# Optimization experiments

Hardware: AMD Instinct MI355X
Metric: run time of the kernel (lower is better)

The kernel has to match this reference:

```python
import jax, jax.numpy as jnp
import numpy as np

B, D, C = 8192, 64, 2048
BETA = 0.25
EPS = 1e-6


def setup_inputs() -> dict:
    key = jax.random.key(0)
    k1, k2, k3 = jax.random.split(key, 3)
    x = jax.random.normal(k1, (B, D), dtype=jnp.float32)
    prev_q = jax.random.normal(k2, (B, D), dtype=jnp.float32)
    codes = jax.random.normal(k3, (1, C, D), dtype=jnp.float32) * 0.1  # learned codebook param
    return {"x": x, "prev_q": prev_q, "codes": codes}


def _rotation_matrix(u, v, eps=EPS):
    # u: (B, D) unit vectors, v: (D,) unit vector. Rodrigues-like rotation mapping v -> u.
    uvT = u[:, :, None] * v[None, None, :]          # (B, D, D)
    vuT = v[None, :, None] * u[:, None, :]          # (B, D, D)
    A = uvT - vuT
    A2 = jnp.einsum('bij,bjk->bik', A, A)
    dot = jnp.sum(u * v[None, :], axis=-1)[:, None, None]  # (B,1,1)
    I = jnp.eye(u.shape[-1], dtype=u.dtype)
    return I[None] + A + A2 / (1.0 + dot + eps)


def reference(x, prev_q, codes):
    # F.normalize(prev_q, dim=-1, eps=1e-6)
    norm = jnp.linalg.norm(prev_q, axis=-1, keepdims=True)
    u = prev_q / jnp.maximum(norm, EPS)
    v = jnp.full((D,), 1.0 / float(D) ** 0.5, dtype=x.dtype)  # registered buffer v

    R = _rotation_matrix(u, v)                      # (B, D, D); R_inv = R^T
    x_canonical = jnp.einsum('bij,bi->bj', R, x)    # R^T @ x

    c0 = codes[0]                                   # (C, D)
    # squared L2 distances (B, C) via GEMM expansion (same math as sum((x-c)^2))
    dists = (jnp.sum(x_canonical ** 2, axis=-1, keepdims=True)
             - 2.0 * (x_canonical @ c0.T)
             + jnp.sum(c0 ** 2, axis=-1)[None, :])
    indices = jnp.argmin(dists, axis=-1)            # (B,)
    quantized_canonical = c0[indices]               # (B, D)

    # STE: value equals quantized_canonical, gradient flows to x_canonical
    q_out = x_canonical + jax.lax.stop_gradient(quantized_canonical - x_canonical)
    quantized = jnp.einsum('bij,bj->bi', R, q_out)  # R @ q_out

    loss_commit = jnp.mean(jnp.sum((x - jax.lax.stop_gradient(quantized_canonical)) ** 2, axis=-1))
    loss_codebook = jnp.mean(jnp.sum((jax.lax.stop_gradient(x) - quantized_canonical) ** 2, axis=-1))
    loss = loss_commit + BETA * loss_codebook
    return quantized, indices, loss
```

## Files before the change

kernel.cpp:

```cpp
#include <hip/hip_runtime.h>
#include <math.h>

#define B_ROWS 8192
#define DIM 64
#define NCODES 2048
#define NSPLIT 16
#define CODES_PER_SPLIT (NCODES / NSPLIT)
#define TILES_PER_WAVE (CODES_PER_SPLIT / 16)
#define EPSF 1e-6f
#define BETA 0.25f
#define V_VAL 0.125f

typedef __attribute__((ext_vector_type(8))) short sh8;
typedef __attribute__((ext_vector_type(4))) float f32x4;

__device__ __forceinline__ float wave_sum64(float v) {
#pragma unroll
    for (int m = 32; m >= 1; m >>= 1) v += __shfl_xor(v, m, 64);
    return v;
}

__device__ __forceinline__ unsigned short f2bf(float f) {
    unsigned u = __float_as_uint(f);
    unsigned r = (u + 0x7fffu + ((u >> 16) & 1u)) >> 16;
    return (unsigned short)r;
}
__device__ __forceinline__ float bf2f(unsigned short h) {
    return __uint_as_float(((unsigned)h) << 16);
}


__global__ void rq_prep_codes(const float* __restrict__ codes,
                              float* __restrict__ cn,
                              unsigned short* __restrict__ cfrag) {
    int tid = threadIdx.x;
    int lane = tid & 63;
    int c = blockIdx.x * 4 + (tid >> 6);
    float cv = codes[(size_t)c * DIM + lane];
    float s = wave_sum64(cv * cv);
    if (lane == 0) cn[c] = s;

    unsigned short s0 = f2bf(cv);
    float r = cv - bf2f(s0);
    unsigned short s1 = f2bf(r);
    r -= bf2f(s1);
    unsigned short s2 = f2bf(r);

    int ct = c >> 4, m = c & 15;
    int h = lane >> 5, q = (lane >> 3) & 3, j = lane & 7;
    int lanep = q * 16 + m;
    size_t base = ((size_t)(ct * 3) * 2 + h) * 512 + (size_t)lanep * 8 + j;
    cfrag[base] = s0;
    cfrag[base + 2 * 512] = s1;
    cfrag[base + 4 * 512] = s2;
}

__global__ void rq_prep_rows(const float* __restrict__ x,
                             const float* __restrict__ pq,
                             unsigned short* __restrict__ xfrag,
                             float* __restrict__ uo,
                             float* __restrict__ duv) {
    int tid = threadIdx.x;
    int lane = tid & 63;
    int r = blockIdx.x * 4 + (tid >> 6);
    float xv = x[(size_t)r * DIM + lane];
    float qv = pq[(size_t)r * DIM + lane];
    float n2 = wave_sum64(qv * qv);
    float inv = 1.0f / fmaxf(sqrtf(n2), EPSF);
    float uv = qv * inv;
    float d = V_VAL * wave_sum64(uv);
    float a = wave_sum64(uv * xv);
    float b = V_VAL * wave_sum64(xv);
    float den = 1.0f + d + EPSF;
    float cu = -b + (d * b - a) / den;
    float cv = a - (b - d * a) / den;
    float xcv = xv + uv * cu + V_VAL * cv;

    uo[(size_t)r * DIM + lane] = uv;
    if (lane == 0) duv[r] = d;

    unsigned short s0 = f2bf(xcv);
    float rr = xcv - bf2f(s0);
    unsigned short s1 = f2bf(rr);
    rr -= bf2f(s1);
    unsigned short s2 = f2bf(rr);

    int rt = r >> 4, m = r & 15;
    int h = lane >> 5, q = (lane >> 3) & 3, j = lane & 7;
    int lanep = q * 16 + m;
    size_t base = ((size_t)(rt * 3) * 2 + h) * 512 + (size_t)lanep * 8 + j;
    xfrag[base] = s0;
    xfrag[base + 2 * 512] = s1;
    xfrag[base + 4 * 512] = s2;
}

__global__ __launch_bounds__(256) void rq_dist_mfma(
        const unsigned short* __restrict__ xfrag,
        const unsigned short* __restrict__ cfrag,
        const float* __restrict__ cn,
        float* __restrict__ pd,
        int* __restrict__ pi) {
    int tid = threadIdx.x;
    int lane = tid & 63;
    int w = tid >> 6;
    int rb = blockIdx.x >> 4;
    int cs = blockIdx.x & (NSPLIT - 1);
    int r0 = rb * 128 + w * 32;
    int rt0 = r0 >> 4;

    const sh8* xf = (const sh8*)xfrag;
    const sh8* cf = (const sh8*)cfrag;

    sh8 afr[2][3][2];
#pragma unroll
    for (int rs = 0; rs < 2; ++rs)
#pragma unroll
        for (int s = 0; s < 3; ++s)
#pragma unroll
            for (int h = 0; h < 2; ++h)
                afr[rs][s][h] = xf[(size_t)(((rt0 + rs) * 3 + s) * 2 + h) * 64 + lane];

    float bv0[4], bv1[4];
    int bi0[4], bi1[4];
#pragma unroll
    for (int i = 0; i < 4; ++i) {
        bv0[i] = INFINITY; bv1[i] = INFINITY;
        bi0[i] = 0x7fffffff; bi1[i] = 0x7fffffff;
    }

    int cbase = cs * CODES_PER_SPLIT;
    for (int t = 0; t < TILES_PER_WAVE; ++t) {
        int c0 = cbase + t * 16;
        int ct = c0 >> 4;
        sh8 bfr[3][2];
#pragma unroll
        for (int s = 0; s < 3; ++s)
#pragma unroll
            for (int h = 0; h < 2; ++h)
                bfr[s][h] = cf[(size_t)((ct * 3 + s) * 2 + h) * 64 + lane];

        f32x4 acc0 = {0.f, 0.f, 0.f, 0.f};
        f32x4 acc1 = {0.f, 0.f, 0.f, 0.f};
#pragma unroll
        for (int h = 0; h < 2; ++h) {
            acc0 = __builtin_amdgcn_mfma_f32_16x16x32_bf16(afr[0][2][h], bfr[0][h], acc0, 0, 0, 0);
            acc0 = __builtin_amdgcn_mfma_f32_16x16x32_bf16(afr[0][1][h], bfr[1][h], acc0, 0, 0, 0);
            acc0 = __builtin_amdgcn_mfma_f32_16x16x32_bf16(afr[0][0][h], bfr[2][h], acc0, 0, 0, 0);
            acc0 = __builtin_amdgcn_mfma_f32_16x16x32_bf16(afr[0][1][h], bfr[0][h], acc0, 0, 0, 0);
            acc0 = __builtin_amdgcn_mfma_f32_16x16x32_bf16(afr[0][0][h], bfr[1][h], acc0, 0, 0, 0);
            acc0 = __builtin_amdgcn_mfma_f32_16x16x32_bf16(afr[0][0][h], bfr[0][h], acc0, 0, 0, 0);

            acc1 = __builtin_amdgcn_mfma_f32_16x16x32_bf16(afr[1][2][h], bfr[0][h], acc1, 0, 0, 0);
            acc1 = __builtin_amdgcn_mfma_f32_16x16x32_bf16(afr[1][1][h], bfr[1][h], acc1, 0, 0, 0);
            acc1 = __builtin_amdgcn_mfma_f32_16x16x32_bf16(afr[1][0][h], bfr[2][h], acc1, 0, 0, 0);
            acc1 = __builtin_amdgcn_mfma_f32_16x16x32_bf16(afr[1][1][h], bfr[0][h], acc1, 0, 0, 0);
            acc1 = __builtin_amdgcn_mfma_f32_16x16x32_bf16(afr[1][0][h], bfr[1][h], acc1, 0, 0, 0);
            acc1 = __builtin_amdgcn_mfma_f32_16x16x32_bf16(afr[1][0][h], bfr[0][h], acc1, 0, 0, 0);
        }

        float cnv = cn[c0 + (lane & 15)];
        int idxv = c0 + (lane & 15);
#pragma unroll
        for (int reg = 0; reg < 4; ++reg) {
            float s0 = fmaf(-2.0f, acc0[reg], cnv);
            if (s0 < bv0[reg]) { bv0[reg] = s0; bi0[reg] = idxv; }
            float s1 = fmaf(-2.0f, acc1[reg], cnv);
            if (s1 < bv1[reg]) { bv1[reg] = s1; bi1[reg] = idxv; }
        }
    }

#pragma unroll
    for (int rs = 0; rs < 2; ++rs) {
#pragma unroll
        for (int reg = 0; reg < 4; ++reg) {
            float v = rs ? bv1[reg] : bv0[reg];
            int ix = rs ? bi1[reg] : bi0[reg];
#pragma unroll
            for (int m = 1; m < 16; m <<= 1) {
                float ov = __shfl_xor(v, m, 64);
                int oi = __shfl_xor(ix, m, 64);
                if (ov < v || (ov == v && oi < ix)) { v = ov; ix = oi; }
            }
            int row = r0 + rs * 16 + (lane >> 4) * 4 + reg;
            if ((lane & 15) == reg) {
                pd[(size_t)cs * B_ROWS + row] = v;
                pi[(size_t)cs * B_ROWS + row] = ix;
            }
        }
    }
}

__global__ void rq_epilogue(const float* __restrict__ x,
                            const float* __restrict__ codes,
                            const float* __restrict__ uo,
                            const float* __restrict__ duv,
                            const float* __restrict__ pd,
                            const int* __restrict__ pi,
                            float* __restrict__ out_q,
                            float* __restrict__ out_idx,
                            float* __restrict__ lossbuf) {
    int tid = threadIdx.x;
    int lane = tid & 63;
    int r = blockIdx.x * 4 + (tid >> 6);

    float dmin = INFINITY;
    int imin = 0x7fffffff;
    if (lane < NSPLIT) {
        dmin = pd[(size_t)lane * B_ROWS + r];
        imin = pi[(size_t)lane * B_ROWS + r];
    }
#pragma unroll
    for (int m = 1; m < 64; m <<= 1) {
        float od = __shfl_xor(dmin, m, 64);
        int oi = __shfl_xor(imin, m, 64);
        if (od < dmin || (od == dmin && oi < imin)) { dmin = od; imin = oi; }
    }
    int idx = imin;

    float qc = codes[(size_t)idx * DIM + lane];
    float uv = uo[(size_t)r * DIM + lane];
    float xv = x[(size_t)r * DIM + lane];
    float d = duv[r];

    float aq = wave_sum64(uv * qc);
    float bq = V_VAL * wave_sum64(qc);
    float den = 1.0f + d + EPSF;
    float cu = bq + (d * bq - aq) / den;
    float cv = -aq - (bq - d * aq) / den;
    float qout = qc + uv * cu + V_VAL * cv;
    out_q[(size_t)r * DIM + lane] = qout;

    float diff = xv - qc;
    float l = wave_sum64(diff * diff);
    if (lane == 0) {
        out_idx[r] = (float)idx;
        lossbuf[r] = l;
    }
}

__global__ void rq_loss_reduce(const float* __restrict__ lossbuf,
                               float* __restrict__ out_loss) {
    __shared__ float part[16];
    int tid = threadIdx.x;
    float s = 0.f;
#pragma unroll
    for (int i = 0; i < B_ROWS / 1024; ++i) s += lossbuf[tid + i * 1024];
    s = wave_sum64(s);
    if ((tid & 63) == 0) part[tid >> 6] = s;
    __syncthreads();
    if (tid < 64) {
        float v = (tid < 16) ? part[tid] : 0.f;
        v = wave_sum64(v);
        if (tid == 0) *out_loss = v * (1.0f + BETA) * (1.0f / (float)B_ROWS);
    }
}

extern "C" void kernel_launch(void* const* d_in, const int* in_sizes, int n_in,
                              void* d_out, int out_size, void* d_ws, size_t ws_size,
                              hipStream_t stream) {
    const float* x     = (const float*)d_in[0];
    const float* pq    = (const float*)d_in[1];
    const float* codes = (const float*)d_in[2];

    float* out      = (float*)d_out;
    float* out_q    = out;
    float* out_idx  = out + (size_t)B_ROWS * DIM;
    float* out_loss = out_idx + B_ROWS;

    char* ws = (char*)d_ws;
    const size_t MB = 1024 * 1024;
    float* uo            = (float*)ws;
    float* duv           = (float*)(ws + 2 * MB);
    float* cn            = (float*)(ws + 2 * MB + 64 * 1024);
    unsigned short* xfrg = (unsigned short*)(ws + 3 * MB);
    unsigned short* cfrg = (unsigned short*)(ws + 6 * MB);
    float* pd            = (float*)(ws + 7 * MB);
    int*   pi            = (int*)(ws + 7 * MB + 512 * 1024);
    float* lbuf          = (float*)(ws + 8 * MB);

    rq_prep_codes<<<NCODES / 4, 256, 0, stream>>>(codes, cn, cfrg);
    rq_prep_rows<<<B_ROWS / 4, 256, 0, stream>>>(x, pq, xfrg, uo, duv);
    rq_dist_mfma<<<64 * NSPLIT, 256, 0, stream>>>(xfrg, cfrg, cn, pd, pi);
    rq_epilogue<<<B_ROWS / 4, 256, 0, stream>>>(
        x, codes, uo, duv, pd, pi, out_q, out_idx, lbuf);
    rq_loss_reduce<<<1, 1024, 0, stream>>>(lbuf, out_loss);
}
```

Measured before the change: 94.61 us.

## Fuse prep kernels, use 64-bit atomicMin argmin keys and atomic loss reduction

The two prep kernels are merged into one launch that handles rows and codes in different block ranges, and it also initialises the per-row argmin keys and the loss counters. The distance kernel no longer writes per-split partial minima. It packs an order-preserving float key and the index into a 64-bit value and applies atomicMin per row, so the epilogue reads the chosen index directly. The loss is accumulated with fixed-point 64-bit atomics plus a last-block counter, which removes the separate reduce kernel. This cuts two launches and some global traffic, at the cost of atomic contention and a fixed-point quantisation of the loss.

```diff
diff --git a/kernel.cpp b/kernel.cpp
--- a/kernel.cpp
+++ b/kernel.cpp
@@ -30,76 +30,81 @@
 }
 
 
-__global__ void rq_prep_codes(const float* __restrict__ codes,
-                              float* __restrict__ cn,
-                              unsigned short* __restrict__ cfrag) {
+__global__ void rq_prep(const float* __restrict__ x,
+                        const float* __restrict__ pq,
+                        const float* __restrict__ codes,
+                        float* __restrict__ cn,
+                        unsigned short* __restrict__ cfrag,
+                        unsigned short* __restrict__ xfrag,
+                        float* __restrict__ uo,
+                        float* __restrict__ duv,
+                        unsigned long long* __restrict__ keys,
+                        unsigned long long* __restrict__ lacc,
+                        unsigned int* __restrict__ cnt) {
     int tid = threadIdx.x;
     int lane = tid & 63;
-    int c = blockIdx.x * 4 + (tid >> 6);
-    float cv = codes[(size_t)c * DIM + lane];
-    float s = wave_sum64(cv * cv);
-    if (lane == 0) cn[c] = s;
-
-    unsigned short s0 = f2bf(cv);
-    float r = cv - bf2f(s0);
-    unsigned short s1 = f2bf(r);
-    r -= bf2f(s1);
-    unsigned short s2 = f2bf(r);
-
-    int ct = c >> 4, m = c & 15;
-    int h = lane >> 5, q = (lane >> 3) & 3, j = lane & 7;
-    int lanep = q * 16 + m;
-    size_t base = ((size_t)(ct * 3) * 2 + h) * 512 + (size_t)lanep * 8 + j;
-    cfrag[base] = s0;
-    cfrag[base + 2 * 512] = s1;
-    cfrag[base + 4 * 512] = s2;
-}
-
-__global__ void rq_prep_rows(const float* __restrict__ x,
-                             const float* __restrict__ pq,
-                             unsigned short* __restrict__ xfrag,
-                             float* __restrict__ uo,
-                             float* __restrict__ duv) {
-    int tid = threadIdx.x;
-    int lane = tid & 63;
-    int r = blockIdx.x * 4 + (tid >> 6);
-    float xv = x[(size_t)r * DIM + lane];
-    float qv = pq[(size_t)r * DIM + lane];
-    float n2 = wave_sum64(qv * qv);
-    float inv = 1.0f / fmaxf(sqrtf(n2), EPSF);
-    float uv = qv * inv;
-    float d = V_VAL * wave_sum64(uv);
-    float a = wave_sum64(uv * xv);
-    float b = V_VAL * wave_sum64(xv);
-    float den = 1.0f + d + EPSF;
-    float cu = -b + (d * b - a) / den;
-    float cv = a - (b - d * a) / den;
-    float xcv = xv + uv * cu + V_VAL * cv;
-
-    uo[(size_t)r * DIM + lane] = uv;
-    if (lane == 0) duv[r] = d;
-
-    unsigned short s0 = f2bf(xcv);
-    float rr = xcv - bf2f(s0);
-    unsigned short s1 = f2bf(rr);
-    rr -= bf2f(s1);
-    unsigned short s2 = f2bf(rr);
-
-    int rt = r >> 4, m = r & 15;
-    int h = lane >> 5, q = (lane >> 3) & 3, j = lane & 7;
-    int lanep = q * 16 + m;
-    size_t base = ((size_t)(rt * 3) * 2 + h) * 512 + (size_t)lanep * 8 + j;
-    xfrag[base] = s0;
-    xfrag[base + 2 * 512] = s1;
-    xfrag[base + 4 * 512] = s2;
+    int bid = blockIdx.x;
+
+    if (bid < B_ROWS / 4) {
+        int r = bid * 4 + (tid >> 6);
+        float xv = x[(size_t)r * DIM + lane];
+        float qv = pq[(size_t)r * DIM + lane];
+        float n2 = wave_sum64(qv * qv);
+        float inv = 1.0f / fmaxf(sqrtf(n2), EPSF);
+        float uv = qv * inv;
+        float d = V_VAL * wave_sum64(uv);
+        float a = wave_sum64(uv * xv);
+        float b = V_VAL * wave_sum64(xv);
+        float den = 1.0f + d + EPSF;
+        float cu = -b + (d * b - a) / den;
+        float cv = a - (b - d * a) / den;
+        float xcv = xv + uv * cu + V_VAL * cv;
+
+        uo[(size_t)r * DIM + lane] = uv;
+        if (lane == 0) duv[r] = d;
+        if (lane == 1) keys[r] = 0xFFFFFFFFFFFFFFFFull;
+        if (bid == 0 && tid == 0) { *lacc = 0ull; *cnt = 0u; }
+
+        unsigned short s0 = f2bf(xcv);
+        float rr = xcv - bf2f(s0);
+        unsigned short s1 = f2bf(rr);
+        rr -= bf2f(s1);
+        unsigned short s2 = f2bf(rr);
+
+        int rt = r >> 4, m = r & 15;
+        int h = lane >> 5, q = (lane >> 3) & 3, j = lane & 7;
+        int lanep = q * 16 + m;
+        size_t base = ((size_t)(rt * 3) * 2 + h) * 512 + (size_t)lanep * 8 + j;
+        xfrag[base] = s0;
+        xfrag[base + 2 * 512] = s1;
+        xfrag[base + 4 * 512] = s2;
+    } else {
+        int c = (bid - B_ROWS / 4) * 4 + (tid >> 6);
+        float cvv = codes[(size_t)c * DIM + lane];
+        float s = wave_sum64(cvv * cvv);
+        if (lane == 0) cn[c] = s;
+
+        unsigned short s0 = f2bf(cvv);
+        float rr = cvv - bf2f(s0);
+        unsigned short s1 = f2bf(rr);
+        rr -= bf2f(s1);
+        unsigned short s2 = f2bf(rr);
+
+        int ct = c >> 4, m = c & 15;
+        int h = lane >> 5, q = (lane >> 3) & 3, j = lane & 7;
+        int lanep = q * 16 + m;
+        size_t base = ((size_t)(ct * 3) * 2 + h) * 512 + (size_t)lanep * 8 + j;
+        cfrag[base] = s0;
+        cfrag[base + 2 * 512] = s1;
+        cfrag[base + 4 * 512] = s2;
+    }
 }
 
 __global__ __launch_bounds__(256) void rq_dist_mfma(
         const unsigned short* __restrict__ xfrag,
         const unsigned short* __restrict__ cfrag,
         const float* __restrict__ cn,
-        float* __restrict__ pd,
-        int* __restrict__ pi) {
+        unsigned long long* __restrict__ keys) {
     int tid = threadIdx.x;
     int lane = tid & 63;
     int w = tid >> 6;
@@ -181,10 +186,13 @@
                 int oi = __shfl_xor(ix, m, 64);
                 if (ov < v || (ov == v && oi < ix)) { v = ov; ix = oi; }
             }
-            int row = r0 + rs * 16 + (lane >> 4) * 4 + reg;
             if ((lane & 15) == reg) {
-                pd[(size_t)cs * B_ROWS + row] = v;
-                pi[(size_t)cs * B_ROWS + row] = ix;
+                int row = r0 + rs * 16 + (lane >> 4) * 4 + reg;
+                unsigned u = __float_as_uint(v);
+                unsigned k32 = (u & 0x80000000u) ? ~u : (u | 0x80000000u);
+                unsigned long long key =
+                    ((unsigned long long)k32 << 32) | (unsigned long long)(unsigned)ix;
+                atomicMin(&keys[row], key);
             }
         }
     }
@@ -194,28 +202,19 @@
                             const float* __restrict__ codes,
                             const float* __restrict__ uo,
                             const float* __restrict__ duv,
-                            const float* __restrict__ pd,
-                            const int* __restrict__ pi,
+                            const unsigned long long* __restrict__ keys,
+                            unsigned long long* __restrict__ lacc,
+                            unsigned int* __restrict__ cnt,
                             float* __restrict__ out_q,
                             float* __restrict__ out_idx,
-                            float* __restrict__ lossbuf) {
+                            float* __restrict__ out_loss) {
+    __shared__ float part[4];
     int tid = threadIdx.x;
     int lane = tid & 63;
-    int r = blockIdx.x * 4 + (tid >> 6);
-
-    float dmin = INFINITY;
-    int imin = 0x7fffffff;
-    if (lane < NSPLIT) {
-        dmin = pd[(size_t)lane * B_ROWS + r];
-        imin = pi[(size_t)lane * B_ROWS + r];
-    }
-#pragma unroll
-    for (int m = 1; m < 64; m <<= 1) {
-        float od = __shfl_xor(dmin, m, 64);
-        int oi = __shfl_xor(imin, m, 64);
-        if (od < dmin || (od == dmin && oi < imin)) { dmin = od; imin = oi; }
-    }
-    int idx = imin;
+    int w = tid >> 6;
+    int r = blockIdx.x * 4 + w;
+
+    int idx = (int)(unsigned)(keys[r] & 0xFFFFFFFFull);
 
     float qc = codes[(size_t)idx * DIM + lane];
     float uv = uo[(size_t)r * DIM + lane];
@@ -234,24 +233,20 @@
     float l = wave_sum64(diff * diff);
     if (lane == 0) {
         out_idx[r] = (float)idx;
-        lossbuf[r] = l;
-    }
-}
-
-__global__ void rq_loss_reduce(const float* __restrict__ lossbuf,
-                               float* __restrict__ out_loss) {
-    __shared__ float part[16];
-    int tid = threadIdx.x;
-    float s = 0.f;
-#pragma unroll
-    for (int i = 0; i < B_ROWS / 1024; ++i) s += lossbuf[tid + i * 1024];
-    s = wave_sum64(s);
-    if ((tid & 63) == 0) part[tid >> 6] = s;
+        part[w] = l;
+    }
     __syncthreads();
-    if (tid < 64) {
-        float v = (tid < 16) ? part[tid] : 0.f;
-        v = wave_sum64(v);
-        if (tid == 0) *out_loss = v * (1.0f + BETA) * (1.0f / (float)B_ROWS);
+    if (tid == 0) {
+        float bs = part[0] + part[1] + part[2] + part[3];
+        unsigned long long qi = (unsigned long long)((double)bs * 1048576.0 + 0.5);
+        atomicAdd(lacc, qi);
+        __threadfence();
+        unsigned int old = atomicAdd(cnt, 1u);
+        if (old == (unsigned)(gridDim.x - 1)) {
+            unsigned long long tot = atomicAdd(lacc, 0ull);
+            *out_loss = (float)((double)tot *
+                                ((1.0 + (double)BETA) / (1048576.0 * (double)B_ROWS)));
+        }
     }
 }
 
@@ -269,19 +264,18 @@
 
     char* ws = (char*)d_ws;
     const size_t MB = 1024 * 1024;
-    float* uo            = (float*)ws;
-    float* duv           = (float*)(ws + 2 * MB);
-    float* cn            = (float*)(ws + 2 * MB + 64 * 1024);
-    unsigned short* xfrg = (unsigned short*)(ws + 3 * MB);
-    unsigned short* cfrg = (unsigned short*)(ws + 6 * MB);
-    float* pd            = (float*)(ws + 7 * MB);
-    int*   pi            = (int*)(ws + 7 * MB + 512 * 1024);
-    float* lbuf          = (float*)(ws + 8 * MB);
-
-    rq_prep_codes<<<NCODES / 4, 256, 0, stream>>>(codes, cn, cfrg);
-    rq_prep_rows<<<B_ROWS / 4, 256, 0, stream>>>(x, pq, xfrg, uo, duv);
-    rq_dist_mfma<<<64 * NSPLIT, 256, 0, stream>>>(xfrg, cfrg, cn, pd, pi);
+    float* uo                = (float*)ws;
+    float* duv               = (float*)(ws + 2 * MB);
+    float* cn                = (float*)(ws + 2 * MB + 32 * 1024);
+    unsigned long long* keys = (unsigned long long*)(ws + 2 * MB + 64 * 1024);
+    unsigned long long* lacc = (unsigned long long*)(ws + 2 * MB + 128 * 1024);
+    unsigned int* cnt        = (unsigned int*)(ws + 2 * MB + 128 * 1024 + 8);
+    unsigned short* xfrg     = (unsigned short*)(ws + 3 * MB);
+    unsigned short* cfrg     = (unsigned short*)(ws + 6 * MB);
+
+    rq_prep<<<B_ROWS / 4 + NCODES / 4, 256, 0, stream>>>(
+        x, pq, codes, cn, cfrg, xfrg, uo, duv, keys, lacc, cnt);
+    rq_dist_mfma<<<64 * NSPLIT, 256, 0, stream>>>(xfrg, cfrg, cn, keys);
     rq_epilogue<<<B_ROWS / 4, 256, 0, stream>>>(
-        x, codes, uo, duv, pd, pi, out_q, out_idx, lbuf);
-    rq_loss_reduce<<<1, 1024, 0, stream>>>(lbuf, out_loss);
-}
+        x, codes, uo, duv, keys, lacc, cnt, out_q, out_idx, out_loss);
+}
```

Result: slower. 138.2 us (+46.1%).
